# Kernel optimization log

Hardware: AMD Instinct MI355X
Metric: run time of the kernel (lower is better)

The kernel has to match this reference:

```python
import jax, jax.numpy as jnp
import numpy as np

N = 50000
E = 800000
NODE_IN, EDGE_IN, HID, OUT, L = 32, 16, 128, 128, 2


def _layer_norm(h, g, b, eps=1e-5):
    mu = jnp.mean(h, axis=-1, keepdims=True)
    var = jnp.var(h, axis=-1, keepdims=True)
    return (h - mu) * jax.lax.rsqrt(var + eps) * g + b


def setup_inputs() -> dict:
    key = jax.random.key(0)
    ks = jax.random.split(key, 20)
    s = lambda k, shape, fan: jax.random.normal(k, shape, jnp.float32) * (1.0 / np.sqrt(fan))
    return {
        "x": jax.random.normal(ks[0], (N, NODE_IN), jnp.float32),
        "edge_index": jax.random.randint(ks[1], (2, E), 0, N, jnp.int64),
        "edge_attr": jax.random.normal(ks[2], (E, EDGE_IN), jnp.float32),
        "enc_W": s(ks[3], (NODE_IN, HID), NODE_IN),
        "enc_b": jnp.zeros((HID,), jnp.float32),
        "enc_g": jnp.ones((HID,), jnp.float32),
        "enc_beta": jnp.zeros((HID,), jnp.float32),
        "msg_W1": s(ks[4], (L, 2 * HID + EDGE_IN, HID), 2 * HID + EDGE_IN),
        "msg_b1": jnp.zeros((L, HID), jnp.float32),
        "msg_W2": s(ks[5], (L, HID, HID), HID),
        "msg_b2": jnp.zeros((L, HID), jnp.float32),
        "upd_W1": s(ks[6], (L, 2 * HID, HID), 2 * HID),
        "upd_b1": jnp.zeros((L, HID), jnp.float32),
        "upd_W2": s(ks[7], (L, HID, HID), HID),
        "upd_b2": jnp.zeros((L, HID), jnp.float32),
        "ln_g": jnp.ones((L, HID), jnp.float32),
        "ln_beta": jnp.zeros((L, HID), jnp.float32),
        "head_W": s(ks[8], (HID, OUT), HID),
        "head_b": jnp.zeros((OUT,), jnp.float32),
    }


def reference(x, edge_index, edge_attr, enc_W, enc_b, enc_g, enc_beta,
              msg_W1, msg_b1, msg_W2, msg_b2, upd_W1, upd_b1, upd_W2, upd_b2,
              ln_g, ln_beta, head_W, head_b):
    src = edge_index[0]  # x_j (source)
    tgt = edge_index[1]  # x_i (target, aggregation index)
    n = x.shape[0]

    # node encoder: Linear -> ReLU -> LayerNorm
    h = jax.nn.relu(x @ enc_W + enc_b)
    h = _layer_norm(h, enc_g, enc_beta)

    # per-edge incoming-degree for mean aggregation (isolated nodes -> 0)
    cnt = jax.ops.segment_sum(jnp.ones((tgt.shape[0],), h.dtype), tgt, num_segments=n)
    denom = jnp.maximum(cnt, 1.0)[:, None]

    for l in range(L):
        x_i = h[tgt]                                 # [E, HID]
        x_j = h[src]                                 # [E, HID]
        msg_in = jnp.concatenate([x_i, x_j, edge_attr], axis=-1)  # [E, 2H+Ed]
        m = jax.nn.relu(msg_in @ msg_W1[l] + msg_b1[l]) @ msg_W2[l] + msg_b2[l]
        aggr = jax.ops.segment_sum(m, tgt, num_segments=n) / denom  # mean
        upd_in = jnp.concatenate([h, aggr], axis=-1)
        out = jax.nn.relu(upd_in @ upd_W1[l] + upd_b1[l]) @ upd_W2[l] + upd_b2[l]
        h = _layer_norm(h + out, ln_g[l], ln_beta[l])

    return h @ head_W + head_b
```

## Files before the change

kernel.cpp:

```cpp
#include <hip/hip_runtime.h>
#include <hip/hip_bf16.h>
#include <stdint.h>

#define N_NODES 50000
#define N_EDGES 800000
#define NL 2

#define KS2 136
#define KSU 264
#define ESTR 133

typedef __bf16 bf16x8 __attribute__((ext_vector_type(8)));
typedef float f32x4 __attribute__((ext_vector_type(4)));

__device__ __forceinline__ f32x4 mfma_bf16(uint4 a, uint4 b, f32x4 c) {
    return __builtin_amdgcn_mfma_f32_16x16x32_bf16(
        __builtin_bit_cast(bf16x8, a), __builtin_bit_cast(bf16x8, b), c, 0, 0, 0);
}

__device__ __forceinline__ unsigned short f2b(float f) {
    union { float f; unsigned u; } v; v.f = f;
    unsigned r = v.u + 0x7FFFu + ((v.u >> 16) & 1u);
    return (unsigned short)(r >> 16);
}

__device__ __forceinline__ float b2f(unsigned short u) {
    union { unsigned u; float f; } v; v.u = ((unsigned)u) << 16; return v.f;
}
__device__ __forceinline__ float b2f_lo(unsigned u) {
    union { unsigned u; float f; } v; v.u = u << 16; return v.f;
}
__device__ __forceinline__ float b2f_hi(unsigned u) {
    union { unsigned u; float f; } v; v.u = u & 0xFFFF0000u; return v.f;
}

template<int KSTEPS, int BSTR>
__device__ __forceinline__ void gemm8(const unsigned short* aLane,
                                      const unsigned short* bLane, f32x4 acc[8]) {
#pragma unroll
    for (int kc = 0; kc < KSTEPS; kc++) {
        uint4 a = *(const uint4*)(aLane + kc * 32);
#pragma unroll
        for (int ct = 0; ct < 8; ct++) {
            uint4 b = *(const uint4*)(bLane + (size_t)ct * 16 * BSTR + kc * 32);
            acc[ct] = mfma_bf16(a, b, acc[ct]);
        }
    }
}

template<int KSTEPS, int ASTR, int BSTR>
__device__ __forceinline__ void gemm_2x4(const unsigned short* aLane,
                                         const unsigned short* bLane,
                                         f32x4 acc[4][2]) {
#pragma unroll
    for (int kc = 0; kc < KSTEPS; kc++) {
        uint4 b0 = *(const uint4*)(bLane + kc * 32);
        uint4 b1 = *(const uint4*)(bLane + (size_t)16 * BSTR + kc * 32);
#pragma unroll
        for (int rt = 0; rt < 4; rt++) {
            uint4 a = *(const uint4*)(aLane + (size_t)rt * 16 * ASTR + kc * 32);
            acc[rt][0] = mfma_bf16(a, b0, acc[rt][0]);
            acc[rt][1] = mfma_bf16(a, b1, acc[rt][1]);
        }
    }
}

__global__ void prep_kernel(const float* __restrict__ mW1,
                            const float* __restrict__ uW1, const float* __restrict__ uW2,
                            const float* __restrict__ hW,
                            unsigned short* __restrict__ wab, unsigned short* __restrict__ w1cp,
                            unsigned short* __restrict__ u1t, unsigned short* __restrict__ u2t,
                            unsigned short* __restrict__ ht) {
    int i = blockIdx.x * 256 + threadIdx.x;
    const int SA = NL * 256 * 136;
    const int SC = NL * 128 * 32;
    const int SU = NL * 128 * KSU;
    const int S3 = NL * 128 * KS2;
    const int S4 = 128 * KS2;
    if (i < SA) {
        int l = i / (256 * 136), r = i % (256 * 136), j = r / 136, k = r % 136;
        float v = 0.f;
        if (k < 128)
            v = (j < 128) ? mW1[((size_t)l * 272 + k) * 128 + j]
                          : mW1[((size_t)l * 272 + 128 + k) * 128 + (j - 128)];
        wab[i] = f2b(v);
        return;
    }
    i -= SA;
    if (i < SC) {
        int l = i / (128 * 32), r = i % (128 * 32), j = r / 32, k = r % 32;
        w1cp[i] = (k < 16) ? f2b(mW1[((size_t)l * 272 + 256 + k) * 128 + j]) : (unsigned short)0;
        return;
    }
    i -= SC;
    if (i < SU) {
        int l = i / (128 * KSU), r = i % (128 * KSU), n = r / KSU, k = r % KSU;
        if (k < 128)       u1t[i] = f2b(uW1[((size_t)l * 256 + k) * 128 + n]);
        else if (k >= 256) u1t[i] = 0;
        return;
    }
    i -= SU;
    if (i < S3) {
        int l = i / (128 * KS2), r = i % (128 * KS2), n = r / KS2, k = r % KS2;
        u2t[i] = (k < 128) ? f2b(uW2[((size_t)l * 128 + k) * 128 + n]) : (unsigned short)0;
        return;
    }
    i -= S3;
    if (i < S4) {
        int n = i / KS2, k = i % KS2;
        ht[i] = (k < 128) ? f2b(hW[(size_t)k * 128 + n]) : (unsigned short)0;
    }
}

__global__ void prep2_kernel(const float* __restrict__ mW2, const float* __restrict__ uW1,
                             unsigned short* __restrict__ u1t) {
    __shared__ float w2row[128];
    const int l = blockIdx.x >> 7, j = blockIdx.x & 127;
    const int n = threadIdx.x;
    w2row[n] = mW2[((size_t)l * 128 + j) * 128 + n];
    __syncthreads();
    float s = 0.f;
#pragma unroll 8
    for (int c = 0; c < 128; c++)
        s += w2row[c] * uW1[((size_t)l * 256 + 128 + c) * 128 + n];
    u1t[(size_t)l * 128 * KSU + (size_t)n * KSU + 128 + j] = f2b(s);
}

__global__ void prep3_kernel(const float* __restrict__ mb2, const float* __restrict__ uW1,
                             float* __restrict__ bfold) {
    const int l = blockIdx.x;
    const int n = threadIdx.x;
    float s = 0.f;
#pragma unroll 8
    for (int c = 0; c < 128; c++)
        s += mb2[l * 128 + c] * uW1[((size_t)l * 256 + 128 + c) * 128 + n];
    bfold[l * 128 + n] = s;
}

__global__ __launch_bounds__(256) void enc_kernel(
        const float* __restrict__ x, const float* __restrict__ W,
        const float* __restrict__ b, const float* __restrict__ g, const float* __restrict__ bet,
        float* __restrict__ h, unsigned short* __restrict__ hb) {
    __shared__ float sx[64];
    __shared__ float redS[4], redSS[4];
    const int t = threadIdx.x;
    const int nb = blockIdx.x * 2;
    if (t < 64) sx[t] = x[(size_t)nb * 32 + t];
    __syncthreads();
    const int half = t >> 7, j = t & 127;
    const int node = nb + half;
    float acc = b[j];
#pragma unroll
    for (int k = 0; k < 32; k++) acc += sx[half * 32 + k] * W[k * 128 + j];
    float v = fmaxf(acc, 0.f);
    float s = v, ss = v * v;
#pragma unroll
    for (int d = 32; d > 0; d >>= 1) { s += __shfl_down(s, d); ss += __shfl_down(ss, d); }
    const int wv = t >> 6;
    if ((t & 63) == 0) { redS[wv] = s; redSS[wv] = ss; }
    __syncthreads();
    float S = redS[half * 2] + redS[half * 2 + 1];
    float SS = redSS[half * 2] + redSS[half * 2 + 1];
    float mu = S * (1.f / 128.f);
    float var = SS * (1.f / 128.f) - mu * mu;
    float rs = rsqrtf(var + 1e-5f);
    float o = (v - mu) * rs * g[j] + bet[j];
    h[(size_t)node * 128 + j] = o;
    hb[(size_t)node * 128 + j] = f2b(o);
}

__global__ void hist_kernel(const int* __restrict__ tgt, int* __restrict__ hist) {
    int i = blockIdx.x * 256 + threadIdx.x;
    atomicAdd(hist + tgt[i], 1);
}

__global__ void scan1_kernel(const int* __restrict__ hist, int* __restrict__ incl,
                             int* __restrict__ blksum) {
    __shared__ int buf[256];
    const int t = threadIdx.x;
    const int i = blockIdx.x * 256 + t;
    int v = (i < N_NODES) ? hist[i] : 0;
    buf[t] = v; __syncthreads();
#pragma unroll
    for (int d = 1; d < 256; d <<= 1) {
        int x = (t >= d) ? buf[t - d] : 0;
        __syncthreads();
        buf[t] += x;
        __syncthreads();
    }
    if (i < N_NODES) incl[i] = buf[t];
    if (t == 255) blksum[blockIdx.x] = buf[255];
}

__global__ void scan2_kernel(int* __restrict__ blksum, int nblk) {
    __shared__ int buf[256];
    const int t = threadIdx.x;
    int v = (t < nblk) ? blksum[t] : 0;
    buf[t] = v; __syncthreads();
#pragma unroll
    for (int d = 1; d < 256; d <<= 1) {
        int x = (t >= d) ? buf[t - d] : 0;
        __syncthreads();
        buf[t] += x;
        __syncthreads();
    }
    if (t < nblk) blksum[t] = buf[t];
}

__global__ void scan3_kernel(int* __restrict__ incl, const int* __restrict__ blksum,
                             const int* __restrict__ hist) {
    const int i = blockIdx.x * 256 + threadIdx.x;
    if (i >= N_NODES) return;
    const int b = blockIdx.x;
    const int base = (b > 0) ? blksum[b - 1] : 0;
    incl[i] = incl[i] + base - hist[i];
}

__global__ void scatterp_kernel(const int* __restrict__ src, const int* __restrict__ tgt,
                                int* __restrict__ cursor, uint2* __restrict__ permst) {
    const int e = blockIdx.x * 256 + threadIdx.x;
    const int tg = tgt[e];
    const int p = atomicAdd(cursor + tg, 1);
    permst[p] = make_uint2((unsigned)e, ((unsigned)src[e] << 16) | (unsigned)tg);
}

__global__ __launch_bounds__(256) void gather_kernel(
        const uint2* __restrict__ permst, const float* __restrict__ ea,
        unsigned int* __restrict__ sST, unsigned short* __restrict__ eabS) {
    const int p = blockIdx.x * 256 + threadIdx.x;
    const uint2 v = permst[p];
    sST[p] = v.y;
    const float4* s = (const float4*)(ea + (size_t)v.x * 16);
    ushort4* d = (ushort4*)(eabS + (size_t)p * 16);
#pragma unroll
    for (int i = 0; i < 4; i++) {
        float4 f = s[i];
        d[i] = make_ushort4(f2b(f.x), f2b(f.y), f2b(f.z), f2b(f.w));
    }
}

__global__ __launch_bounds__(256, 4) void node_kernel(
        const unsigned short* __restrict__ hb, const unsigned short* __restrict__ wab,
        const float* __restrict__ b1,
        unsigned short* __restrict__ Tb, unsigned short* __restrict__ Sb) {
    __shared__ __align__(16) unsigned short As[64 * KS2];
    const int t = threadIdx.x;
    const int n0 = blockIdx.x * 64;
    {
        const int m = t >> 2, q = t & 3;
        const int node = n0 + m;
        uint4* dst = (uint4*)(As + m * KS2);
        if (node < N_NODES) {
            const uint4* s = (const uint4*)(hb + (size_t)node * 128);
#pragma unroll
            for (int i = 0; i < 4; i++) dst[q * 4 + i] = s[q * 4 + i];
        } else {
            uint4 z{0, 0, 0, 0};
            for (int i = q; i < 16; i += 4) dst[i] = z;
        }
    }
    __syncthreads();

    const int wv = t >> 6, lane = t & 63, lr = lane & 15, lq = lane >> 4;
    const int cb = wv * 64;
    const f32x4 z4 = {0.f, 0.f, 0.f, 0.f};
    f32x4 acc[4][4];
#pragma unroll
    for (int i = 0; i < 4; i++)
#pragma unroll
        for (int j = 0; j < 4; j++) acc[i][j] = z4;

    const unsigned short* aL = As + lr * KS2 + lq * 8;
    const unsigned short* bL = wab + (size_t)(cb + lr) * KS2 + lq * 8;
#pragma unroll
    for (int kc = 0; kc < 4; kc++) {
        uint4 bA = *(const uint4*)(bL + kc * 32);
        uint4 bB = *(const uint4*)(bL + (size_t)16 * KS2 + kc * 32);
        uint4 bC = *(const uint4*)(bL + (size_t)32 * KS2 + kc * 32);
        uint4 bD = *(const uint4*)(bL + (size_t)48 * KS2 + kc * 32);
#pragma unroll
        for (int rt = 0; rt < 4; rt++) {
            uint4 a = *(const uint4*)(aL + (size_t)rt * 16 * KS2 + kc * 32);
            acc[rt][0] = mfma_bf16(a, bA, acc[rt][0]);
            acc[rt][1] = mfma_bf16(a, bB, acc[rt][1]);
            acc[rt][2] = mfma_bf16(a, bC, acc[rt][2]);
            acc[rt][3] = mfma_bf16(a, bD, acc[rt][3]);
        }
    }
#pragma unroll
    for (int ct = 0; ct < 4; ct++) {
        const int j = cb + ct * 16 + lr;
        const float bias = (j < 128) ? b1[j] : 0.f;
#pragma unroll
        for (int rt = 0; rt < 4; rt++) {
#pragma unroll
            for (int r = 0; r < 4; r++) {
                const int node = n0 + rt * 16 + lq * 4 + r;
                if (node < N_NODES) {
                    const float v = acc[rt][ct][r] + bias;
                    if (j < 128) Tb[(size_t)node * 128 + j] = f2b(v);
                    else         Sb[(size_t)node * 128 + (j - 128)] = f2b(v);
                }
            }
        }
    }
}

__global__ __launch_bounds__(256, 8) void edge_kernel(
        const unsigned short* __restrict__ eabS,
        const unsigned int* __restrict__ sST,
        const unsigned short* __restrict__ w1cp,
        const unsigned short* __restrict__ Tb, const unsigned short* __restrict__ Sb,
        float* __restrict__ aggr) {
    __shared__ __align__(16) float Es[32 * ESTR];
    __shared__ int sT[64];
    __shared__ int sS[64];

    const int t = threadIdx.x;
    const int e0 = blockIdx.x * 64;
    if (t < 64) {
        const unsigned v = sST[e0 + t];
        sT[t] = (int)(v & 0xFFFFu);
        sS[t] = (int)(v >> 16);
    }

    const int wv = t >> 6, lane = t & 63, lr = lane & 15, lq = lane >> 4;
    const int rtw = (wv >> 1) * 16;
    const int cbw = (wv & 1) * 64;
    const f32x4 z4 = {0.f, 0.f, 0.f, 0.f};

    unsigned long long bmask = 0ULL;
    float s = 0.f;
    bool first = true;

#pragma unroll
    for (int h = 0; h < 2; h++) {
        if (h) __syncthreads();

        {
            uint4 a = {0, 0, 0, 0};
            if (lq < 2)
                a = *(const uint4*)(eabS + (size_t)(e0 + h * 32 + rtw + lr) * 16 + lq * 8);
            f32x4 acc[4];
#pragma unroll
            for (int ct = 0; ct < 4; ct++) {
                uint4 b = *(const uint4*)(w1cp + (cbw + ct * 16 + lr) * 32 + lq * 8);
                acc[ct] = mfma_bf16(a, b, z4);
            }
#pragma unroll
            for (int ct = 0; ct < 4; ct++) {
                const int col = cbw + ct * 16 + lr;
#pragma unroll
                for (int r = 0; r < 4; r++)
                    Es[(rtw + lq * 4 + r) * ESTR + col] = acc[ct][r];
            }
        }
        __syncthreads();

        if (h == 0) {
            const int l = t & 63;
            const int a = sT[l];
            const int b = (l > 0) ? sT[l - 1] : a;
            bmask = __ballot(a != b);
        }

        {
            const int m = t & 31;
            const int c8b = t >> 5;
            const int ge = h * 32 + m;
            const unsigned short* Trow = Tb + (size_t)sT[ge] * 128;
            const unsigned short* Srow = Sb + (size_t)sS[ge] * 128;
            float* Erow = Es + m * ESTR;
#pragma unroll
            for (int it = 0; it < 2; it++) {
                const int c0 = (c8b + it * 8) * 8;
                const uint4 tv = *(const uint4*)(Trow + c0);
                const uint4 sv = *(const uint4*)(Srow + c0);
                float tf[8] = {b2f_lo(tv.x), b2f_hi(tv.x), b2f_lo(tv.y), b2f_hi(tv.y),
                               b2f_lo(tv.z), b2f_hi(tv.z), b2f_lo(tv.w), b2f_hi(tv.w)};
                float sf[8] = {b2f_lo(sv.x), b2f_hi(sv.x), b2f_lo(sv.y), b2f_hi(sv.y),
                               b2f_lo(sv.z), b2f_hi(sv.z), b2f_lo(sv.w), b2f_hi(sv.w)};
#pragma unroll
                for (int i = 0; i < 8; i++)
                    Erow[c0 + i] = fmaxf(Erow[c0 + i] + tf[i] + sf[i], 0.f);
            }
        }
        __syncthreads();

        if (t < 128) {
            const int c = t;
            const unsigned mh = (unsigned)(bmask >> (h * 32));
#pragma unroll
            for (int i = 0; i < 32; i++) {
                if (mh & (1u << i)) {
                    float* dst = aggr + (size_t)sT[h * 32 + i - 1] * 128 + c;
                    if (first) { atomicAdd(dst, s); first = false; }
                    else       { *dst = s; }
                    s = 0.f;
                }
                s += Es[i * ESTR + c];
            }
        }
    }
    if (t < 128) atomicAdd(aggr + (size_t)sT[63] * 128 + t, s);
}

__global__ __launch_bounds__(256, 4) void upd_kernel(
        const unsigned short* __restrict__ hb_in, const float* __restrict__ h_in,
        const float* __restrict__ aggr, const int* __restrict__ hist,
        const unsigned short* __restrict__ u1t, const unsigned short* __restrict__ u2t,
        const float* __restrict__ b1, const float* __restrict__ bf,
        const float* __restrict__ b2,
        const float* __restrict__ g, const float* __restrict__ bet,
        float* __restrict__ h_out, unsigned short* __restrict__ hb_out) {
    __shared__ __align__(16) char smemA[64 * KSU * 2];
    __shared__ float sF[64];
    unsigned short* As = (unsigned short*)smemA;
    float* LNb = (float*)smemA;

    const int t = threadIdx.x;
    const int n0 = blockIdx.x * 64;
    {
        const int m = t >> 2, q = t & 3;
        const int node = n0 + m;
        unsigned short* row = As + m * KSU;
        if (node < N_NODES) {
            const uint4* ph = (const uint4*)(hb_in + (size_t)node * 128);
            uint4* d0 = (uint4*)row;
#pragma unroll
            for (int i = 0; i < 4; i++) d0[q * 4 + i] = ph[q * 4 + i];
            const int cntv = hist[node];
            if (q == 0) sF[m] = (cntv > 0) ? 1.f : 0.f;
            const float rden = 1.0f / fmaxf((float)cntv, 1.0f);
            const float4* pa = (const float4*)(aggr + (size_t)node * 128 + q * 32);
            ushort4* d1 = (ushort4*)(row + 128 + q * 32);
#pragma unroll
            for (int i = 0; i < 8; i++) {
                float4 v = pa[i];
                d1[i] = make_ushort4(f2b(v.x * rden), f2b(v.y * rden),
                                     f2b(v.z * rden), f2b(v.w * rden));
            }
            if (q == 0) { uint4 z{0, 0, 0, 0}; ((uint4*)(row + 256))[0] = z; }
        } else {
            if (q == 0) sF[m] = 0.f;
            uint4 z{0, 0, 0, 0};
            uint4* d = (uint4*)row;
            for (int i = q; i < 33; i += 4) d[i] = z;
        }
    }
    __syncthreads();

    const int wv = t >> 6, lane = t & 63, lr = lane & 15, lq = lane >> 4;
    const int cb = wv * 32;
    const f32x4 z4 = {0.f, 0.f, 0.f, 0.f};

    f32x4 acc[4][2];
#pragma unroll
    for (int i = 0; i < 4; i++) { acc[i][0] = z4; acc[i][1] = z4; }
    gemm_2x4<8, KSU, KSU>(As + lr * KSU + lq * 8,
                          u1t + (size_t)(cb + lr) * KSU + lq * 8, acc);
    __syncthreads();

#pragma unroll
    for (int ct = 0; ct < 2; ct++) {
        const int col = cb + ct * 16 + lr;
        const float bv = b1[col];
        const float bfv = bf[col];
#pragma unroll
        for (int rt = 0; rt < 4; rt++) {
#pragma unroll
            for (int r = 0; r < 4; r++) {
                const int ml = rt * 16 + lq * 4 + r;
                float v = fmaxf(acc[rt][ct][r] + bv + sF[ml] * bfv, 0.f);
                As[ml * KSU + col] = f2b(v);
            }
        }
    }
    __syncthreads();

    f32x4 acc2[4][2];
#pragma unroll
    for (int i = 0; i < 4; i++) { acc2[i][0] = z4; acc2[i][1] = z4; }
    gemm_2x4<4, KSU, KS2>(As + lr * KSU + lq * 8,
                          u2t + (size_t)(cb + lr) * KS2 + lq * 8, acc2);
    __syncthreads();

#pragma unroll
    for (int ct = 0; ct < 2; ct++) {
        const int col = cb + ct * 16 + lr;
        const float bv = b2[col];
#pragma unroll
        for (int rt = 0; rt < 4; rt++) {
#pragma unroll
            for (int r = 0; r < 4; r++) {
                const int ml = rt * 16 + lq * 4 + r;
                const int node = n0 + ml;
                if (node < N_NODES)
                    LNb[ml * 132 + col] = acc2[rt][ct][r] + bv + h_in[(size_t)node * 128 + col];
            }
        }
    }
    __syncthreads();

    {
        const int r = t >> 2, c0 = (t & 3) * 32;
        const int node = n0 + r;
        if (node < N_NODES) {
            float s = 0.f, ss = 0.f;
#pragma unroll
            for (int i = 0; i < 32; i++) { float v = LNb[r * 132 + c0 + i]; s += v; ss += v * v; }
            s += __shfl_xor(s, 1); ss += __shfl_xor(ss, 1);
            s += __shfl_xor(s, 2); ss += __shfl_xor(ss, 2);
            const float mu = s * (1.0f / 128.0f);
            const float var = ss * (1.0f / 128.0f) - mu * mu;
            const float rs = rsqrtf(var + 1e-5f);
#pragma unroll
            for (int i = 0; i < 32; i++) {
                const int j = c0 + i;
                float v = (LNb[r * 132 + j] - mu) * rs * g[j] + bet[j];
                h_out[(size_t)node * 128 + j] = v;
                hb_out[(size_t)node * 128 + j] = f2b(v);
            }
        }
    }
}

__global__ __launch_bounds__(256, 2) void head_kernel(
        const unsigned short* __restrict__ hb, const unsigned short* __restrict__ ht,
        const float* __restrict__ hbias, float* __restrict__ out) {
    __shared__ __align__(16) unsigned short As[64 * KS2];
    const int t = threadIdx.x;
    const int n0 = blockIdx.x * 64;
    {
        const int m = t >> 2, q = t & 3;
        const int node = n0 + m;
        uint4* dst = (uint4*)(As + m * KS2);
        if (node < N_NODES) {
            const uint4* s = (const uint4*)(hb + (size_t)node * 128);
#pragma unroll
            for (int i = 0; i < 4; i++) dst[q * 4 + i] = s[q * 4 + i];
        } else {
            uint4 z{0, 0, 0, 0};
            for (int i = q; i < 16; i += 4) dst[i] = z;
        }
    }
    __syncthreads();

    const int wv = t >> 6, lane = t & 63, lr = lane & 15, lq = lane >> 4;
    const int m0 = wv * 16;
    const f32x4 z4 = {0.f, 0.f, 0.f, 0.f};
    f32x4 acc[8];
#pragma unroll
    for (int i = 0; i < 8; i++) acc[i] = z4;
    gemm8<4, KS2>(As + (m0 + lr) * KS2 + lq * 8, ht + (size_t)lr * KS2 + lq * 8, acc);
#pragma unroll
    for (int ct = 0; ct < 8; ct++) {
        const int col = ct * 16 + lr;
        const float bv = hbias[col];
#pragma unroll
        for (int r = 0; r < 4; r++) {
            const int node = n0 + m0 + lq * 4 + r;
            if (node < N_NODES) out[(size_t)node * 128 + col] = acc[ct][r] + bv;
        }
    }
}

extern "C" void kernel_launch(void* const* d_in, const int* in_sizes, int n_in,
                              void* d_out, int out_size, void* d_ws, size_t ws_size,
                              hipStream_t stream) {
    const float* x       = (const float*)d_in[0];
    const int*   ei      = (const int*)d_in[1];
    const float* ea      = (const float*)d_in[2];
    const float* encW    = (const float*)d_in[3];
    const float* encb    = (const float*)d_in[4];
    const float* encg    = (const float*)d_in[5];
    const float* encbeta = (const float*)d_in[6];
    const float* msgW1   = (const float*)d_in[7];
    const float* msgb1   = (const float*)d_in[8];
    const float* msgW2   = (const float*)d_in[9];
    const float* msgb2   = (const float*)d_in[10];
    const float* updW1   = (const float*)d_in[11];
    const float* updb1   = (const float*)d_in[12];
    const float* updW2   = (const float*)d_in[13];
    const float* updb2   = (const float*)d_in[14];
    const float* lng     = (const float*)d_in[15];
    const float* lnbeta  = (const float*)d_in[16];
    const float* headW   = (const float*)d_in[17];
    const float* headb   = (const float*)d_in[18];

    char* w = (char*)d_ws;
    size_t off = 0;
    auto nxt = [&](size_t bytes) -> void* {
        void* p = w + off;
        off = (off + bytes + 255) & ~(size_t)255;
        return p;
    };
    float*          h     = (float*)nxt((size_t)N_NODES * 128 * 4);
    unsigned short* hb    = (unsigned short*)nxt((size_t)N_NODES * 128 * 2);
    float*          aggr  = (float*)nxt((size_t)N_NODES * 128 * 4);
    unsigned short* Tb    = (unsigned short*)nxt((size_t)N_NODES * 128 * 2);
    unsigned short* Sb    = (unsigned short*)nxt((size_t)N_NODES * 128 * 2);
    unsigned short* eabS  = (unsigned short*)nxt((size_t)N_EDGES * 16 * 2);
    unsigned int*   sST   = (unsigned int*)nxt((size_t)N_EDGES * 4);
    int*            hist  = (int*)nxt((size_t)N_NODES * 4);
    int*            incl  = (int*)nxt((size_t)N_NODES * 4);
    int*            blksum= (int*)nxt(256 * 4);
    unsigned short* wab   = (unsigned short*)nxt((size_t)NL * 256 * 136 * 2);
    unsigned short* w1cp  = (unsigned short*)nxt((size_t)NL * 128 * 32 * 2);
    unsigned short* u1t   = (unsigned short*)nxt((size_t)NL * 128 * KSU * 2);
    unsigned short* u2t   = (unsigned short*)nxt((size_t)NL * 128 * KS2 * 2);
    unsigned short* ht    = (unsigned short*)nxt((size_t)128 * KS2 * 2);
    float*          bfold = (float*)nxt((size_t)NL * 128 * 4);

    uint2*          permst = (uint2*)aggr;

    const int NBLK = (N_NODES + 255) / 256;
    const int PREP_N = NL * 256 * 136 + NL * 128 * 32 + NL * 128 * KSU
                     + NL * 128 * KS2 + 128 * KS2;

    hipMemsetAsync(hist, 0, (size_t)N_NODES * 4, stream);
    prep_kernel<<<(PREP_N + 255) / 256, 256, 0, stream>>>(msgW1, updW1, updW2, headW,
                                                          wab, w1cp, u1t, u2t, ht);
    prep2_kernel<<<NL * 128, 128, 0, stream>>>(msgW2, updW1, u1t);
    prep3_kernel<<<NL, 128, 0, stream>>>(msgb2, updW1, bfold);
    enc_kernel<<<25000, 256, 0, stream>>>(x, encW, encb, encg, encbeta, h, hb);
    hist_kernel<<<3125, 256, 0, stream>>>(ei + N_EDGES, hist);
    scan1_kernel<<<NBLK, 256, 0, stream>>>(hist, incl, blksum);
    scan2_kernel<<<1, 256, 0, stream>>>(blksum, NBLK);
    scan3_kernel<<<NBLK, 256, 0, stream>>>(incl, blksum, hist);
    scatterp_kernel<<<3125, 256, 0, stream>>>(ei, ei + N_EDGES, incl, permst);
    gather_kernel<<<3125, 256, 0, stream>>>(permst, ea, sST, eabS);

    for (int l = 0; l < NL; l++) {
        node_kernel<<<782, 256, 0, stream>>>(hb, wab + (size_t)l * 256 * 136,
                                             msgb1 + l * 128, Tb, Sb);
        hipMemsetAsync(aggr, 0, (size_t)N_NODES * 128 * 4, stream);
        edge_kernel<<<12500, 256, 0, stream>>>(eabS, sST,
                                               w1cp + (size_t)l * 128 * 32,
                                               Tb, Sb, aggr);
        upd_kernel<<<782, 256, 0, stream>>>(hb, h, aggr, hist,
                                            u1t + (size_t)l * 128 * KSU,
                                            u2t + (size_t)l * 128 * KS2,
                                            updb1 + l * 128, bfold + l * 128,
                                            updb2 + l * 128,
                                            lng + l * 128, lnbeta + l * 128, h, hb);
    }
    head_kernel<<<782, 256, 0, stream>>>(hb, ht, headb, (float*)d_out);
}
```

Before: 558.3 us.

## Prefetch edge gathers ahead of MFMA and vectorize LDS accesses in edge kernel

The two-half loop in the edge kernel is unrolled by hand, and the bf16 T/S row gathers for each half are issued early: the first half's rows load before the edge-attribute MFMA, and the second half's load during the first half's ReLU pass. The LDS row stride changes from 133 to 132 so rows can be read and written as float4. The segmented reduction now batches 8 LDS reads before the scan. This aims to hide gather latency and cut LDS instruction count, at the cost of more registers held live and possible LDS bank conflicts from the power-of-two-aligned stride.

```diff
diff --git a/kernel.cpp b/kernel.cpp
--- a/kernel.cpp
+++ b/kernel.cpp
@@ -8,7 +8,7 @@
 
 #define KS2 136
 #define KSU 264
-#define ESTR 133
+#define ESTR 132
 
 typedef __bf16 bf16x8 __attribute__((ext_vector_type(8)));
 typedef float f32x4 __attribute__((ext_vector_type(4)));
@@ -323,86 +323,182 @@
         sT[t] = (int)(v & 0xFFFFu);
         sS[t] = (int)(v >> 16);
     }
+    __syncthreads();
 
     const int wv = t >> 6, lane = t & 63, lr = lane & 15, lq = lane >> 4;
     const int rtw = (wv >> 1) * 16;
     const int cbw = (wv & 1) * 64;
+    const int m = t & 31, c8b = t >> 5;
     const f32x4 z4 = {0.f, 0.f, 0.f, 0.f};
 
-    unsigned long long bmask = 0ULL;
+    unsigned long long bmask;
+    {
+        const int l = t & 63;
+        const int a = sT[l];
+        const int b = (l > 0) ? sT[l - 1] : a;
+        bmask = __ballot(a != b);
+    }
+
+    uint4 t0a, t0b, s0a, s0b;
+    {
+        const unsigned short* Tr = Tb + (size_t)sT[m] * 128;
+        const unsigned short* Sr = Sb + (size_t)sS[m] * 128;
+        t0a = *(const uint4*)(Tr + c8b * 8);
+        t0b = *(const uint4*)(Tr + c8b * 8 + 64);
+        s0a = *(const uint4*)(Sr + c8b * 8);
+        s0b = *(const uint4*)(Sr + c8b * 8 + 64);
+    }
+
     float s = 0.f;
     bool first = true;
 
-#pragma unroll
-    for (int h = 0; h < 2; h++) {
-        if (h) __syncthreads();
-
-        {
-            uint4 a = {0, 0, 0, 0};
-            if (lq < 2)
-                a = *(const uint4*)(eabS + (size_t)(e0 + h * 32 + rtw + lr) * 16 + lq * 8);
-            f32x4 acc[4];
-#pragma unroll
-            for (int ct = 0; ct < 4; ct++) {
-                uint4 b = *(const uint4*)(w1cp + (cbw + ct * 16 + lr) * 32 + lq * 8);
-                acc[ct] = mfma_bf16(a, b, z4);
-            }
-#pragma unroll
-            for (int ct = 0; ct < 4; ct++) {
-                const int col = cbw + ct * 16 + lr;
-#pragma unroll
-                for (int r = 0; r < 4; r++)
-                    Es[(rtw + lq * 4 + r) * ESTR + col] = acc[ct][r];
-            }
-        }
-        __syncthreads();
-
-        if (h == 0) {
-            const int l = t & 63;
-            const int a = sT[l];
-            const int b = (l > 0) ? sT[l - 1] : a;
-            bmask = __ballot(a != b);
-        }
-
-        {
-            const int m = t & 31;
-            const int c8b = t >> 5;
-            const int ge = h * 32 + m;
-            const unsigned short* Trow = Tb + (size_t)sT[ge] * 128;
-            const unsigned short* Srow = Sb + (size_t)sS[ge] * 128;
-            float* Erow = Es + m * ESTR;
-#pragma unroll
-            for (int it = 0; it < 2; it++) {
-                const int c0 = (c8b + it * 8) * 8;
-                const uint4 tv = *(const uint4*)(Trow + c0);
-                const uint4 sv = *(const uint4*)(Srow + c0);
-                float tf[8] = {b2f_lo(tv.x), b2f_hi(tv.x), b2f_lo(tv.y), b2f_hi(tv.y),
-                               b2f_lo(tv.z), b2f_hi(tv.z), b2f_lo(tv.w), b2f_hi(tv.w)};
-                float sf[8] = {b2f_lo(sv.x), b2f_hi(sv.x), b2f_lo(sv.y), b2f_hi(sv.y),
-                               b2f_lo(sv.z), b2f_hi(sv.z), b2f_lo(sv.w), b2f_hi(sv.w)};
-#pragma unroll
-                for (int i = 0; i < 8; i++)
-                    Erow[c0 + i] = fmaxf(Erow[c0 + i] + tf[i] + sf[i], 0.f);
-            }
-        }
-        __syncthreads();
-
-        if (t < 128) {
-            const int c = t;
-            const unsigned mh = (unsigned)(bmask >> (h * 32));
-#pragma unroll
-            for (int i = 0; i < 32; i++) {
+    {
+        uint4 a = {0, 0, 0, 0};
+        if (lq < 2)
+            a = *(const uint4*)(eabS + (size_t)(e0 + rtw + lr) * 16 + lq * 8);
+        f32x4 acc[4];
+#pragma unroll
+        for (int ct = 0; ct < 4; ct++) {
+            uint4 b = *(const uint4*)(w1cp + (cbw + ct * 16 + lr) * 32 + lq * 8);
+            acc[ct] = mfma_bf16(a, b, z4);
+        }
+#pragma unroll
+        for (int ct = 0; ct < 4; ct++) {
+            const int col = cbw + ct * 16 + lr;
+#pragma unroll
+            for (int r = 0; r < 4; r++)
+                Es[(rtw + lq * 4 + r) * ESTR + col] = acc[ct][r];
+        }
+    }
+    __syncthreads();
+
+    uint4 t1a, t1b, s1a, s1b;
+    {
+        float* Erow = Es + m * ESTR;
+        float4* EA = (float4*)(Erow + c8b * 8);
+        float4* EB = (float4*)(Erow + c8b * 8 + 64);
+        float4 ea0 = EA[0], ea1 = EA[1];
+        ea0.x = fmaxf(ea0.x + b2f_lo(t0a.x) + b2f_lo(s0a.x), 0.f);
+        ea0.y = fmaxf(ea0.y + b2f_hi(t0a.x) + b2f_hi(s0a.x), 0.f);
+        ea0.z = fmaxf(ea0.z + b2f_lo(t0a.y) + b2f_lo(s0a.y), 0.f);
+        ea0.w = fmaxf(ea0.w + b2f_hi(t0a.y) + b2f_hi(s0a.y), 0.f);
+        ea1.x = fmaxf(ea1.x + b2f_lo(t0a.z) + b2f_lo(s0a.z), 0.f);
+        ea1.y = fmaxf(ea1.y + b2f_hi(t0a.z) + b2f_hi(s0a.z), 0.f);
+        ea1.z = fmaxf(ea1.z + b2f_lo(t0a.w) + b2f_lo(s0a.w), 0.f);
+        ea1.w = fmaxf(ea1.w + b2f_hi(t0a.w) + b2f_hi(s0a.w), 0.f);
+        EA[0] = ea0; EA[1] = ea1;
+        float4 eb0 = EB[0], eb1 = EB[1];
+        eb0.x = fmaxf(eb0.x + b2f_lo(t0b.x) + b2f_lo(s0b.x), 0.f);
+        eb0.y = fmaxf(eb0.y + b2f_hi(t0b.x) + b2f_hi(s0b.x), 0.f);
+        eb0.z = fmaxf(eb0.z + b2f_lo(t0b.y) + b2f_lo(s0b.y), 0.f);
+        eb0.w = fmaxf(eb0.w + b2f_hi(t0b.y) + b2f_hi(s0b.y), 0.f);
+        eb1.x = fmaxf(eb1.x + b2f_lo(t0b.z) + b2f_lo(s0b.z), 0.f);
+        eb1.y = fmaxf(eb1.y + b2f_hi(t0b.z) + b2f_hi(s0b.z), 0.f);
+        eb1.z = fmaxf(eb1.z + b2f_lo(t0b.w) + b2f_lo(s0b.w), 0.f);
+        eb1.w = fmaxf(eb1.w + b2f_hi(t0b.w) + b2f_hi(s0b.w), 0.f);
+        EB[0] = eb0; EB[1] = eb1;
+
+        const unsigned short* Tr = Tb + (size_t)sT[32 + m] * 128;
+        const unsigned short* Sr = Sb + (size_t)sS[32 + m] * 128;
+        t1a = *(const uint4*)(Tr + c8b * 8);
+        t1b = *(const uint4*)(Tr + c8b * 8 + 64);
+        s1a = *(const uint4*)(Sr + c8b * 8);
+        s1b = *(const uint4*)(Sr + c8b * 8 + 64);
+    }
+    __syncthreads();
+
+    if (t < 128) {
+        const int c = t;
+        const unsigned mh = (unsigned)bmask;
+#pragma unroll
+        for (int i8 = 0; i8 < 4; i8++) {
+            float v[8];
+#pragma unroll
+            for (int j = 0; j < 8; j++) v[j] = Es[(i8 * 8 + j) * ESTR + c];
+#pragma unroll
+            for (int j = 0; j < 8; j++) {
+                const int i = i8 * 8 + j;
                 if (mh & (1u << i)) {
-                    float* dst = aggr + (size_t)sT[h * 32 + i - 1] * 128 + c;
+                    float* dst = aggr + (size_t)sT[i - 1] * 128 + c;
                     if (first) { atomicAdd(dst, s); first = false; }
                     else       { *dst = s; }
                     s = 0.f;
                 }
-                s += Es[i * ESTR + c];
+                s += v[j];
             }
         }
     }
-    if (t < 128) atomicAdd(aggr + (size_t)sT[63] * 128 + t, s);
+    __syncthreads();
+
+    {
+        uint4 a = {0, 0, 0, 0};
+        if (lq < 2)
+            a = *(const uint4*)(eabS + (size_t)(e0 + 32 + rtw + lr) * 16 + lq * 8);
+        f32x4 acc[4];
+#pragma unroll
+        for (int ct = 0; ct < 4; ct++) {
+            uint4 b = *(const uint4*)(w1cp + (cbw + ct * 16 + lr) * 32 + lq * 8);
+            acc[ct] = mfma_bf16(a, b, z4);
+        }
+#pragma unroll
+        for (int ct = 0; ct < 4; ct++) {
+            const int col = cbw + ct * 16 + lr;
+#pragma unroll
+            for (int r = 0; r < 4; r++)
+                Es[(rtw + lq * 4 + r) * ESTR + col] = acc[ct][r];
+        }
+    }
+    __syncthreads();
+
+    {
+        float* Erow = Es + m * ESTR;
+        float4* EA = (float4*)(Erow + c8b * 8);
+        float4* EB = (float4*)(Erow + c8b * 8 + 64);
+        float4 ea0 = EA[0], ea1 = EA[1];
+        ea0.x = fmaxf(ea0.x + b2f_lo(t1a.x) + b2f_lo(s1a.x), 0.f);
+        ea0.y = fmaxf(ea0.y + b2f_hi(t1a.x) + b2f_hi(s1a.x), 0.f);
+        ea0.z = fmaxf(ea0.z + b2f_lo(t1a.y) + b2f_lo(s1a.y), 0.f);
+        ea0.w = fmaxf(ea0.w + b2f_hi(t1a.y) + b2f_hi(s1a.y), 0.f);
+        ea1.x = fmaxf(ea1.x + b2f_lo(t1a.z) + b2f_lo(s1a.z), 0.f);
+        ea1.y = fmaxf(ea1.y + b2f_hi(t1a.z) + b2f_hi(s1a.z), 0.f);
+        ea1.z = fmaxf(ea1.z + b2f_lo(t1a.w) + b2f_lo(s1a.w), 0.f);
+        ea1.w = fmaxf(ea1.w + b2f_hi(t1a.w) + b2f_hi(s1a.w), 0.f);
+        EA[0] = ea0; EA[1] = ea1;
+        float4 eb0 = EB[0], eb1 = EB[1];
+        eb0.x = fmaxf(eb0.x + b2f_lo(t1b.x) + b2f_lo(s1b.x), 0.f);
+        eb0.y = fmaxf(eb0.y + b2f_hi(t1b.x) + b2f_hi(s1b.x), 0.f);
+        eb0.z = fmaxf(eb0.z + b2f_lo(t1b.y) + b2f_lo(s1b.y), 0.f);
+        eb0.w = fmaxf(eb0.w + b2f_hi(t1b.y) + b2f_hi(s1b.y), 0.f);
+        eb1.x = fmaxf(eb1.x + b2f_lo(t1b.z) + b2f_lo(s1b.z), 0.f);
+        eb1.y = fmaxf(eb1.y + b2f_hi(t1b.z) + b2f_hi(s1b.z), 0.f);
+        eb1.z = fmaxf(eb1.z + b2f_lo(t1b.w) + b2f_lo(s1b.w), 0.f);
+        eb1.w = fmaxf(eb1.w + b2f_hi(t1b.w) + b2f_hi(s1b.w), 0.f);
+        EB[0] = eb0; EB[1] = eb1;
+    }
+    __syncthreads();
+
+    if (t < 128) {
+        const int c = t;
+        const unsigned mh = (unsigned)(bmask >> 32);
+#pragma unroll
+        for (int i8 = 0; i8 < 4; i8++) {
+            float v[8];
+#pragma unroll
+            for (int j = 0; j < 8; j++) v[j] = Es[(i8 * 8 + j) * ESTR + c];
+#pragma unroll
+            for (int j = 0; j < 8; j++) {
+                const int i = i8 * 8 + j;
+                if (mh & (1u << i)) {
+                    float* dst = aggr + (size_t)sT[32 + i - 1] * 128 + c;
+                    if (first) { atomicAdd(dst, s); first = false; }
+                    else       { *dst = s; }
+                    s = 0.f;
+                }
+                s += v[j];
+            }
+        }
+        atomicAdd(aggr + (size_t)sT[63] * 128 + c, s);
+    }
 }
 
 __global__ __launch_bounds__(256, 4) void upd_kernel(
```

Result: no change. 550.5 us (-1.4%).
